# Kernel tuning notes

Measured on AMD Instinct MI355X. Metric: run time of the kernel, lower is better.

## Reference

```python
import jax, jax.numpy as jnp
import numpy as np

T, B, F, H = 128, 32768, 8, 64


def gru_step(h, x, Wih, Whh, bih, bhh):
    # PyTorch GRU cell, gate order (r, z, n)
    gi = x @ Wih.T + bih          # [B, 3H]
    gh = h @ Whh.T + bhh          # [B, 3H]
    i_r, i_z, i_n = jnp.split(gi, 3, axis=-1)
    h_r, h_z, h_n = jnp.split(gh, 3, axis=-1)
    r = jax.nn.sigmoid(i_r + h_r)
    z = jax.nn.sigmoid(i_z + h_z)
    n = jnp.tanh(i_n + r * h_n)
    return (1.0 - z) * n + z * h


def setup_inputs() -> dict:
    key = jax.random.key(0)
    ks = jax.random.split(key, 12)
    s = 0.1  # small init scale
    return {
        "inputs": jax.random.normal(ks[0], (T, B, F), jnp.float32),
        "target": jax.random.normal(ks[1], (T, B, F), jnp.float32),
        "enc_Wih": jax.random.normal(ks[2], (3 * H, F), jnp.float32) * s,
        "enc_Whh": jax.random.normal(ks[3], (3 * H, H), jnp.float32) * s,
        "enc_bih": jax.random.normal(ks[4], (3 * H,), jnp.float32) * s,
        "enc_bhh": jax.random.normal(ks[5], (3 * H,), jnp.float32) * s,
        "dec_Wih": jax.random.normal(ks[6], (3 * H, F), jnp.float32) * s,
        "dec_Whh": jax.random.normal(ks[7], (3 * H, H), jnp.float32) * s,
        "dec_bih": jax.random.normal(ks[8], (3 * H,), jnp.float32) * s,
        "dec_bhh": jax.random.normal(ks[9], (3 * H,), jnp.float32) * s,
        "out_W": jax.random.normal(ks[10], (F, H), jnp.float32) * s,
        "out_b": jax.random.normal(ks[11], (F,), jnp.float32) * s,
    }


def reference(inputs, target, enc_Wih, enc_Whh, enc_bih, enc_bhh,
              dec_Wih, dec_Whh, dec_bih, dec_bhh, out_W, out_b):
    batch = inputs.shape[1]
    # ---- Encoder: single-layer GRU over T steps, h0 = 0 ----
    h0 = jnp.zeros((batch, H), inputs.dtype)

    def enc_body(h, x_t):
        h = gru_step(h, x_t, enc_Wih, enc_Whh, enc_bih, enc_bhh)
        return h, None

    enc_hidden, _ = jax.lax.scan(enc_body, h0, inputs)

    # ---- Decoder: teacher forcing; input at t=0 is zeros, then target[t-1] ----
    dec_in = jnp.concatenate(
        [jnp.zeros((1, batch, target.shape[2]), target.dtype), target[:-1]], axis=0)

    def dec_body(h, x_t):
        h = gru_step(h, x_t, dec_Wih, dec_Whh, dec_bih, dec_bhh)
        y = h @ out_W.T + out_b  # [B, F]
        return h, y

    _, decoder_outputs = jax.lax.scan(dec_body, enc_hidden, dec_in)
    return decoder_outputs  # [T, B, F]
```

## Files before the change

### kernel.cpp

```cpp
#include <hip/hip_runtime.h>

#define T_STEPS 128
#define B_SIZE  32768
#define F_DIM   8
#define H_DIM   64

#define BLOCK_THREADS 128
#define GRID_BLOCKS   (B_SIZE / 16)

typedef float f32x4 __attribute__((ext_vector_type(4)));
typedef short bfrag __attribute__((ext_vector_type(8)));
typedef unsigned int u32x4 __attribute__((ext_vector_type(4)));

#define MFMA16(A, B, C) __builtin_amdgcn_mfma_f32_16x16x32_bf16((A), (B), (C), 0, 0, 0)

#define LDS_BARRIER() asm volatile("s_waitcnt lgkmcnt(0)\n\ts_barrier" ::: "memory")

__device__ __forceinline__ short f2bf(float f) { return __builtin_bit_cast(short, (__bf16)f); }
__device__ __forceinline__ float4 ld4(const void* p) { return *(const float4*)p; }

constexpr float S1 = 1.4426950408889634f;
constexpr float S2 = 2.f * S1;


__global__ void __launch_bounds__(BLOCK_THREADS, 2)
seq2seq_r9_kernel(const float* __restrict__ inputs, const float* __restrict__ target,
                  const float* __restrict__ eWih, const float* __restrict__ eWhh,
                  const float* __restrict__ ebih, const float* __restrict__ ebhh,
                  const float* __restrict__ dWih, const float* __restrict__ dWhh,
                  const float* __restrict__ dbih, const float* __restrict__ dbhh,
                  const float* __restrict__ oW, const float* __restrict__ ob,
                  float* __restrict__ out)
{
    __shared__ u32x4 sEx[2][2][64];

    const int tid  = threadIdx.x;
    const int lane = tid & 63;
    const int w    = tid >> 6;
    const int c    = lane & 15;
    const int g    = lane >> 4;

    bfrag wr[2][2], wz[2][2], whn[2][2];
    bfrag xr[2], xz[2], xnw[2];
    f32x4 bhn[2];

    auto load_phase = [&](const float* __restrict__ Wih, const float* __restrict__ Whh,
                          const float* __restrict__ bih, const float* __restrict__ bhh) {
#pragma unroll
        for (int tl = 0; tl < 2; ++tl) {
            const int tt = 2 * w + tl;
            const int rowR = 16 * tt + c, rowZ = rowR + 64, rowN = rowR + 128;
#pragma unroll
            for (int j = 0; j < 2; ++j) {
                const int kt = (j == 0) ? w : 1 - w;
                bfrag fr, fz, fn;
#pragma unroll
                for (int e = 0; e < 8; ++e) {
                    const int k = 32 * kt + 16 * (e >> 2) + 4 * g + (e & 3);
                    fr[e] = f2bf(Whh[rowR * H_DIM + k] * S1);
                    fz[e] = f2bf(Whh[rowZ * H_DIM + k] * S1);
                    fn[e] = f2bf(Whh[rowN * H_DIM + k] * S2);
                }
                wr[tl][j] = fr; wz[tl][j] = fz; whn[tl][j] = fn;
            }
            bfrag axr, axz, axn;
#pragma unroll
            for (int e = 0; e < 8; ++e) {
                const int k = 16 * (e >> 2) + 4 * g + (e & 3);
                float vr = 0.f, vz = 0.f, vn = 0.f;
                if (k < F_DIM) {
                    vr = Wih[rowR * F_DIM + k]; vz = Wih[rowZ * F_DIM + k]; vn = Wih[rowN * F_DIM + k];
                } else if (k == F_DIM) {
                    vr = bih[rowR] + bhh[rowR]; vz = bih[rowZ] + bhh[rowZ]; vn = bih[rowN];
                }
                axr[e] = f2bf(vr * S1); axz[e] = f2bf(vz * S1); axn[e] = f2bf(vn * S2);
            }
            xr[tl] = axr; xz[tl] = axz; xnw[tl] = axn;
#pragma unroll
            for (int r4 = 0; r4 < 4; ++r4) bhn[tl][r4] = bhh[128 + 16 * tt + 4 * g + r4] * S2;
        }
    };

    f32x4 hc[2] = {{0.f,0.f,0.f,0.f},{0.f,0.f,0.f,0.f}};
    bfrag hl = (bfrag){0,0,0,0,0,0,0,0};
    bfrag ho = (bfrag){0,0,0,0,0,0,0,0};
    bfrag bx0 = (bfrag){0,0,0,0,0,0,0,0};
    if (g == 2) bx0[0] = f2bf(1.f);

    auto step = [&](const bfrag bx) {
#pragma unroll
        for (int tl = 0; tl < 2; ++tl) {
            f32x4 aIN = {0.f,0.f,0.f,0.f};
            aIN = MFMA16(xnw[tl], bx, aIN);
            f32x4 aR = {0.f,0.f,0.f,0.f};
            aR = MFMA16(xr[tl], bx, aR);
            aR = MFMA16(wr[tl][0], hl, aR);
            f32x4 aZ = {0.f,0.f,0.f,0.f};
            aZ = MFMA16(xz[tl], bx, aZ);
            aZ = MFMA16(wz[tl][0], hl, aZ);
            f32x4 aHN = bhn[tl];
            aHN = MFMA16(whn[tl][0], hl, aHN);
            aR  = MFMA16(wr[tl][1],  ho, aR);
            aZ  = MFMA16(wz[tl][1],  ho, aZ);
            aHN = MFMA16(whn[tl][1], ho, aHN);
#pragma unroll
            for (int r4 = 0; r4 < 4; ++r4) {
                const float rg = __builtin_amdgcn_rcpf(1.f + __builtin_amdgcn_exp2f(-aR[r4]));
                const float zg = __builtin_amdgcn_rcpf(1.f + __builtin_amdgcn_exp2f(-aZ[r4]));
                const float np = aIN[r4] + rg * aHN[r4];
                const float ng = 1.f - 2.f * __builtin_amdgcn_rcpf(__builtin_amdgcn_exp2f(np) + 1.f);
                hc[tl][r4] = ng + zg * (hc[tl][r4] - ng);
            }
        }
        bfrag nl;
#pragma unroll
        for (int e = 0; e < 8; ++e) nl[e] = f2bf(hc[e >> 2][e & 3]);
        hl = nl;
    };

    auto make_bx = [&](const float4 xv) {
        bfrag bx = bx0;
        if (g < 2) { bx[0] = f2bf(xv.x); bx[1] = f2bf(xv.y); bx[2] = f2bf(xv.z); bx[3] = f2bf(xv.w); }
        return bx;
    };

    const unsigned istep = B_SIZE * F_DIM * 4;
    const unsigned off0  = ((unsigned)(blockIdx.x * 16 + c) * F_DIM + 4 * g) * 4;

    load_phase(eWih, eWhh, ebih, ebhh);
    __syncthreads();
    float4 xn = make_float4(0.f, 0.f, 0.f, 0.f);
    if (g < 2) xn = ld4((const char*)inputs + off0);
    unsigned ioff = off0 + istep;

    auto enc_body = [&](const int P, const int t) {
        const float4 xv = xn;
        if (g < 2 && t + 1 < T_STEPS) xn = ld4((const char*)inputs + ioff);
        ioff += istep;
        step(make_bx(xv));
        sEx[P][w][lane] = __builtin_bit_cast(u32x4, hl);
        LDS_BARRIER();
        ho = __builtin_bit_cast(bfrag, sEx[P][w ^ 1][lane]);
    };
#pragma unroll 1
    for (int t = 0; t < T_STEPS; t += 2) {
        enc_body(0, t);
        enc_body(1, t + 1);
    }

    load_phase(dWih, dWhh, dbih, dbhh);
    bfrag wo_own, wo_oth;
    f32x4 obv;
#pragma unroll
    for (int j = 0; j < 2; ++j) {
        bfrag f;
#pragma unroll
        for (int e = 0; e < 8; ++e) {
            const int k = 32 * ((j == 0) ? w : 1 - w) + 16 * (e >> 2) + 4 * g + (e & 3);
            f[e] = f2bf((c < F_DIM) ? oW[c * H_DIM + k] : 0.f);
        }
        if (j == 0) wo_own = f; else wo_oth = f;
    }
#pragma unroll
    for (int r4 = 0; r4 < 4; ++r4) obv[r4] = (g < 2) ? ob[4 * g + r4] : 0.f;

    unsigned toff = off0;
    unsigned ooff = off0;
    xn = make_float4(0.f, 0.f, 0.f, 0.f);

    auto dec_body = [&](const int P, const int t) {
        const float4 xv = xn;
        if (g < 2 && t + 1 < T_STEPS) xn = ld4((const char*)target + toff);
        toff += istep;
        step(make_bx(xv));
        sEx[P][w][lane] = __builtin_bit_cast(u32x4, hl);
        LDS_BARRIER();
        ho = __builtin_bit_cast(bfrag, sEx[P][w ^ 1][lane]);
        if (((t + w) & 1) == 0) {
            f32x4 aO = obv;
            aO = MFMA16(wo_own, hl, aO);
            aO = MFMA16(wo_oth, ho, aO);
            if (g < 2) {
                float4 o; o.x = aO[0]; o.y = aO[1]; o.z = aO[2]; o.w = aO[3];
                *(float4*)((char*)out + ooff) = o;
            }
        }
        ooff += istep;
    };
#pragma unroll 1
    for (int t = 0; t < T_STEPS; t += 2) {
        dec_body(0, t);
        dec_body(1, t + 1);
    }
}

extern "C" void kernel_launch(void* const* d_in, const int* in_sizes, int n_in,
                              void* d_out, int out_size, void* d_ws, size_t ws_size,
                              hipStream_t stream) {
    (void)in_sizes; (void)n_in; (void)d_ws; (void)ws_size; (void)out_size;
    const float* inputs = (const float*)d_in[0];
    const float* target = (const float*)d_in[1];
    const float* eWih   = (const float*)d_in[2];
    const float* eWhh   = (const float*)d_in[3];
    const float* ebih   = (const float*)d_in[4];
    const float* ebhh   = (const float*)d_in[5];
    const float* dWih   = (const float*)d_in[6];
    const float* dWhh   = (const float*)d_in[7];
    const float* dbih   = (const float*)d_in[8];
    const float* dbhh   = (const float*)d_in[9];
    const float* oW     = (const float*)d_in[10];
    const float* ob     = (const float*)d_in[11];
    float* out = (float*)d_out;

    seq2seq_r9_kernel<<<dim3(GRID_BLOCKS), dim3(BLOCK_THREADS), 0, stream>>>(
        inputs, target, eWih, eWhh, ebih, ebhh, dWih, dWhh, dbih, dbhh, oW, ob, out);
}
```

Before: 534.6 us.

## Split GRU gate rows across four waves, two batch groups per block

Each block now runs four waves over 32 batch rows in two groups. Each wave owns one 16-row gate tile of the hidden state and processes both batch groups, where before two waves each owned two tiles of a 16-row block. This halves the per-wave weight-fragment registers and interleaves two independent recurrence chains to hide MFMA and transcendental latency. The cost is a full 4-wave __syncthreads per step instead of a 2-wave barrier, and more LDS exchange traffic. The output-projection weights move to LDS and the output step rotates across waves.

```diff
diff --git a/kernel.cpp b/kernel.cpp
--- a/kernel.cpp
+++ b/kernel.cpp
@@ -5,16 +5,16 @@
 #define F_DIM   8
 #define H_DIM   64
 
-#define BLOCK_THREADS 128
-#define GRID_BLOCKS   (B_SIZE / 16)
+#define BLOCK_THREADS 256
+#define GRID_BLOCKS   (B_SIZE / 32)
 
 typedef float f32x4 __attribute__((ext_vector_type(4)));
 typedef short bfrag __attribute__((ext_vector_type(8)));
+typedef short s16x4 __attribute__((ext_vector_type(4)));
+typedef unsigned int u32x2 __attribute__((ext_vector_type(2)));
 typedef unsigned int u32x4 __attribute__((ext_vector_type(4)));
 
 #define MFMA16(A, B, C) __builtin_amdgcn_mfma_f32_16x16x32_bf16((A), (B), (C), 0, 0, 0)
-
-#define LDS_BARRIER() asm volatile("s_waitcnt lgkmcnt(0)\n\ts_barrier" ::: "memory")
 
 __device__ __forceinline__ short f2bf(float f) { return __builtin_bit_cast(short, (__bf16)f); }
 __device__ __forceinline__ float4 ld4(const void* p) { return *(const float4*)p; }
@@ -24,7 +24,7 @@
 
 
 __global__ void __launch_bounds__(BLOCK_THREADS, 2)
-seq2seq_r9_kernel(const float* __restrict__ inputs, const float* __restrict__ target,
+seq2seq_q4_kernel(const float* __restrict__ inputs, const float* __restrict__ target,
                   const float* __restrict__ eWih, const float* __restrict__ eWhh,
                   const float* __restrict__ ebih, const float* __restrict__ ebhh,
                   const float* __restrict__ dWih, const float* __restrict__ dWhh,
@@ -32,91 +32,56 @@
                   const float* __restrict__ oW, const float* __restrict__ ob,
                   float* __restrict__ out)
 {
-    __shared__ u32x4 sEx[2][2][64];
+    __shared__ u32x2 sEx[2][2][2][64][2];
+    __shared__ u32x4 sWo[2][64];
 
     const int tid  = threadIdx.x;
     const int lane = tid & 63;
-    const int w    = tid >> 6;
+    const int q    = tid >> 6;
     const int c    = lane & 15;
     const int g    = lane >> 4;
-
-    bfrag wr[2][2], wz[2][2], whn[2][2];
-    bfrag xr[2], xz[2], xnw[2];
-    f32x4 bhn[2];
+    const int kq   = q >> 1;
+    const int hq   = q & 1;
+
+    bfrag wr[2], wz[2], whn[2];
+    bfrag xr, xz, xnw;
+    f32x4 bhn;
 
     auto load_phase = [&](const float* __restrict__ Wih, const float* __restrict__ Whh,
                           const float* __restrict__ bih, const float* __restrict__ bhh) {
-#pragma unroll
-        for (int tl = 0; tl < 2; ++tl) {
-            const int tt = 2 * w + tl;
-            const int rowR = 16 * tt + c, rowZ = rowR + 64, rowN = rowR + 128;
-#pragma unroll
-            for (int j = 0; j < 2; ++j) {
-                const int kt = (j == 0) ? w : 1 - w;
-                bfrag fr, fz, fn;
-#pragma unroll
-                for (int e = 0; e < 8; ++e) {
-                    const int k = 32 * kt + 16 * (e >> 2) + 4 * g + (e & 3);
-                    fr[e] = f2bf(Whh[rowR * H_DIM + k] * S1);
-                    fz[e] = f2bf(Whh[rowZ * H_DIM + k] * S1);
-                    fn[e] = f2bf(Whh[rowN * H_DIM + k] * S2);
-                }
-                wr[tl][j] = fr; wz[tl][j] = fz; whn[tl][j] = fn;
+        const int rowR = 16 * q + c, rowZ = rowR + 64, rowN = rowR + 128;
+#pragma unroll
+        for (int kt = 0; kt < 2; ++kt) {
+            bfrag fr, fz, fn;
+#pragma unroll
+            for (int e = 0; e < 8; ++e) {
+                const int k = 32 * kt + 16 * (e >> 2) + 4 * g + (e & 3);
+                fr[e] = f2bf(Whh[rowR * H_DIM + k] * S1);
+                fz[e] = f2bf(Whh[rowZ * H_DIM + k] * S1);
+                fn[e] = f2bf(Whh[rowN * H_DIM + k] * S2);
             }
-            bfrag axr, axz, axn;
-#pragma unroll
-            for (int e = 0; e < 8; ++e) {
-                const int k = 16 * (e >> 2) + 4 * g + (e & 3);
-                float vr = 0.f, vz = 0.f, vn = 0.f;
-                if (k < F_DIM) {
-                    vr = Wih[rowR * F_DIM + k]; vz = Wih[rowZ * F_DIM + k]; vn = Wih[rowN * F_DIM + k];
-                } else if (k == F_DIM) {
-                    vr = bih[rowR] + bhh[rowR]; vz = bih[rowZ] + bhh[rowZ]; vn = bih[rowN];
-                }
-                axr[e] = f2bf(vr * S1); axz[e] = f2bf(vz * S1); axn[e] = f2bf(vn * S2);
+            wr[kt] = fr; wz[kt] = fz; whn[kt] = fn;
+        }
+#pragma unroll
+        for (int e = 0; e < 8; ++e) {
+            const int k = 16 * (e >> 2) + 4 * g + (e & 3);
+            float vr = 0.f, vz = 0.f, vn = 0.f;
+            if (k < F_DIM) {
+                vr = Wih[rowR * F_DIM + k]; vz = Wih[rowZ * F_DIM + k]; vn = Wih[rowN * F_DIM + k];
+            } else if (k == F_DIM) {
+                vr = bih[rowR] + bhh[rowR]; vz = bih[rowZ] + bhh[rowZ]; vn = bih[rowN];
             }
-            xr[tl] = axr; xz[tl] = axz; xnw[tl] = axn;
-#pragma unroll
-            for (int r4 = 0; r4 < 4; ++r4) bhn[tl][r4] = bhh[128 + 16 * tt + 4 * g + r4] * S2;
-        }
+            xr[e] = f2bf(vr * S1); xz[e] = f2bf(vz * S1); xnw[e] = f2bf(vn * S2);
+        }
+#pragma unroll
+        for (int r4 = 0; r4 < 4; ++r4) bhn[r4] = bhh[128 + 16 * q + 4 * g + r4] * S2;
     };
 
     f32x4 hc[2] = {{0.f,0.f,0.f,0.f},{0.f,0.f,0.f,0.f}};
-    bfrag hl = (bfrag){0,0,0,0,0,0,0,0};
-    bfrag ho = (bfrag){0,0,0,0,0,0,0,0};
+    bfrag hB[2][2] = {{(bfrag){0,0,0,0,0,0,0,0},(bfrag){0,0,0,0,0,0,0,0}},
+                      {(bfrag){0,0,0,0,0,0,0,0},(bfrag){0,0,0,0,0,0,0,0}}};
     bfrag bx0 = (bfrag){0,0,0,0,0,0,0,0};
     if (g == 2) bx0[0] = f2bf(1.f);
-
-    auto step = [&](const bfrag bx) {
-#pragma unroll
-        for (int tl = 0; tl < 2; ++tl) {
-            f32x4 aIN = {0.f,0.f,0.f,0.f};
-            aIN = MFMA16(xnw[tl], bx, aIN);
-            f32x4 aR = {0.f,0.f,0.f,0.f};
-            aR = MFMA16(xr[tl], bx, aR);
-            aR = MFMA16(wr[tl][0], hl, aR);
-            f32x4 aZ = {0.f,0.f,0.f,0.f};
-            aZ = MFMA16(xz[tl], bx, aZ);
-            aZ = MFMA16(wz[tl][0], hl, aZ);
-            f32x4 aHN = bhn[tl];
-            aHN = MFMA16(whn[tl][0], hl, aHN);
-            aR  = MFMA16(wr[tl][1],  ho, aR);
-            aZ  = MFMA16(wz[tl][1],  ho, aZ);
-            aHN = MFMA16(whn[tl][1], ho, aHN);
-#pragma unroll
-            for (int r4 = 0; r4 < 4; ++r4) {
-                const float rg = __builtin_amdgcn_rcpf(1.f + __builtin_amdgcn_exp2f(-aR[r4]));
-                const float zg = __builtin_amdgcn_rcpf(1.f + __builtin_amdgcn_exp2f(-aZ[r4]));
-                const float np = aIN[r4] + rg * aHN[r4];
-                const float ng = 1.f - 2.f * __builtin_amdgcn_rcpf(__builtin_amdgcn_exp2f(np) + 1.f);
-                hc[tl][r4] = ng + zg * (hc[tl][r4] - ng);
-            }
-        }
-        bfrag nl;
-#pragma unroll
-        for (int e = 0; e < 8; ++e) nl[e] = f2bf(hc[e >> 2][e & 3]);
-        hl = nl;
-    };
 
     auto make_bx = [&](const float4 xv) {
         bfrag bx = bx0;
@@ -124,23 +89,59 @@
         return bx;
     };
 
+    auto step = [&](const bfrag bx, const bfrag hB0, const bfrag hB1, f32x4& HC) -> u32x2 {
+        f32x4 aIN = {0.f,0.f,0.f,0.f};
+        aIN = MFMA16(xnw, bx, aIN);
+        f32x4 aR = {0.f,0.f,0.f,0.f};
+        aR = MFMA16(xr, bx, aR);
+        aR = MFMA16(wr[0], hB0, aR);
+        aR = MFMA16(wr[1], hB1, aR);
+        f32x4 aZ = {0.f,0.f,0.f,0.f};
+        aZ = MFMA16(xz, bx, aZ);
+        aZ = MFMA16(wz[0], hB0, aZ);
+        aZ = MFMA16(wz[1], hB1, aZ);
+        f32x4 aHN = bhn;
+        aHN = MFMA16(whn[0], hB0, aHN);
+        aHN = MFMA16(whn[1], hB1, aHN);
+        s16x4 nb;
+#pragma unroll
+        for (int r4 = 0; r4 < 4; ++r4) {
+            const float rg = __builtin_amdgcn_rcpf(1.f + __builtin_amdgcn_exp2f(-aR[r4]));
+            const float zg = __builtin_amdgcn_rcpf(1.f + __builtin_amdgcn_exp2f(-aZ[r4]));
+            const float np = aIN[r4] + rg * aHN[r4];
+            const float ng = 1.f - 2.f * __builtin_amdgcn_rcpf(__builtin_amdgcn_exp2f(np) + 1.f);
+            HC[r4] = ng + zg * (HC[r4] - ng);
+            nb[r4] = f2bf(HC[r4]);
+        }
+        return __builtin_bit_cast(u32x2, nb);
+    };
+
     const unsigned istep = B_SIZE * F_DIM * 4;
-    const unsigned off0  = ((unsigned)(blockIdx.x * 16 + c) * F_DIM + 4 * g) * 4;
+    const unsigned offg[2] = {
+        ((unsigned)(blockIdx.x * 32 + c) * F_DIM + 4 * g) * 4u,
+        ((unsigned)(blockIdx.x * 32 + 16 + c) * F_DIM + 4 * g) * 4u };
 
     load_phase(eWih, eWhh, ebih, ebhh);
     __syncthreads();
-    float4 xn = make_float4(0.f, 0.f, 0.f, 0.f);
-    if (g < 2) xn = ld4((const char*)inputs + off0);
-    unsigned ioff = off0 + istep;
+    float4 xn[2] = {make_float4(0.f,0.f,0.f,0.f), make_float4(0.f,0.f,0.f,0.f)};
+    if (g < 2) { xn[0] = ld4((const char*)inputs + offg[0]); xn[1] = ld4((const char*)inputs + offg[1]); }
+    unsigned ioff = istep;
 
     auto enc_body = [&](const int P, const int t) {
-        const float4 xv = xn;
-        if (g < 2 && t + 1 < T_STEPS) xn = ld4((const char*)inputs + ioff);
+#pragma unroll
+        for (int grp = 0; grp < 2; ++grp) {
+            const float4 xv = xn[grp];
+            if (g < 2 && t + 1 < T_STEPS) xn[grp] = ld4((const char*)inputs + ioff + offg[grp]);
+            const u32x2 nl = step(make_bx(xv), hB[grp][0], hB[grp][1], hc[grp]);
+            sEx[P][grp][kq][lane][hq] = nl;
+        }
         ioff += istep;
-        step(make_bx(xv));
-        sEx[P][w][lane] = __builtin_bit_cast(u32x4, hl);
-        LDS_BARRIER();
-        ho = __builtin_bit_cast(bfrag, sEx[P][w ^ 1][lane]);
+        __syncthreads();
+#pragma unroll
+        for (int grp = 0; grp < 2; ++grp) {
+            hB[grp][0] = __builtin_bit_cast(bfrag, *(const u32x4*)&sEx[P][grp][0][lane][0]);
+            hB[grp][1] = __builtin_bit_cast(bfrag, *(const u32x4*)&sEx[P][grp][1][lane][0]);
+        }
     };
 #pragma unroll 1
     for (int t = 0; t < T_STEPS; t += 2) {
@@ -148,41 +149,55 @@
         enc_body(1, t + 1);
     }
 
+    __syncthreads();
     load_phase(dWih, dWhh, dbih, dbhh);
-    bfrag wo_own, wo_oth;
+    if (q < 2) {
+        u32x4 f;
+        bfrag bf_;
+#pragma unroll
+        for (int e = 0; e < 8; ++e) {
+            const int k = 32 * q + 16 * (e >> 2) + 4 * g + (e & 3);
+            bf_[e] = f2bf((c < F_DIM) ? oW[c * H_DIM + k] : 0.f);
+        }
+        f = __builtin_bit_cast(u32x4, bf_);
+        sWo[q][lane] = f;
+    }
     f32x4 obv;
 #pragma unroll
-    for (int j = 0; j < 2; ++j) {
-        bfrag f;
-#pragma unroll
-        for (int e = 0; e < 8; ++e) {
-            const int k = 32 * ((j == 0) ? w : 1 - w) + 16 * (e >> 2) + 4 * g + (e & 3);
-            f[e] = f2bf((c < F_DIM) ? oW[c * H_DIM + k] : 0.f);
-        }
-        if (j == 0) wo_own = f; else wo_oth = f;
-    }
-#pragma unroll
     for (int r4 = 0; r4 < 4; ++r4) obv[r4] = (g < 2) ? ob[4 * g + r4] : 0.f;
-
-    unsigned toff = off0;
-    unsigned ooff = off0;
-    xn = make_float4(0.f, 0.f, 0.f, 0.f);
+    __syncthreads();
+
+    unsigned toff = 0;
+    unsigned ooff = 0;
+    xn[0] = xn[1] = make_float4(0.f, 0.f, 0.f, 0.f);
 
     auto dec_body = [&](const int P, const int t) {
-        const float4 xv = xn;
-        if (g < 2 && t + 1 < T_STEPS) xn = ld4((const char*)target + toff);
+#pragma unroll
+        for (int grp = 0; grp < 2; ++grp) {
+            const float4 xv = xn[grp];
+            if (g < 2 && t + 1 < T_STEPS) xn[grp] = ld4((const char*)target + toff + offg[grp]);
+            const u32x2 nl = step(make_bx(xv), hB[grp][0], hB[grp][1], hc[grp]);
+            sEx[P][grp][kq][lane][hq] = nl;
+        }
         toff += istep;
-        step(make_bx(xv));
-        sEx[P][w][lane] = __builtin_bit_cast(u32x4, hl);
-        LDS_BARRIER();
-        ho = __builtin_bit_cast(bfrag, sEx[P][w ^ 1][lane]);
-        if (((t + w) & 1) == 0) {
-            f32x4 aO = obv;
-            aO = MFMA16(wo_own, hl, aO);
-            aO = MFMA16(wo_oth, ho, aO);
-            if (g < 2) {
-                float4 o; o.x = aO[0]; o.y = aO[1]; o.z = aO[2]; o.w = aO[3];
-                *(float4*)((char*)out + ooff) = o;
+        __syncthreads();
+#pragma unroll
+        for (int grp = 0; grp < 2; ++grp) {
+            hB[grp][0] = __builtin_bit_cast(bfrag, *(const u32x4*)&sEx[P][grp][0][lane][0]);
+            hB[grp][1] = __builtin_bit_cast(bfrag, *(const u32x4*)&sEx[P][grp][1][lane][0]);
+        }
+        if ((t & 3) == q) {
+            const bfrag wo0 = __builtin_bit_cast(bfrag, sWo[0][lane]);
+            const bfrag wo1 = __builtin_bit_cast(bfrag, sWo[1][lane]);
+#pragma unroll
+            for (int grp = 0; grp < 2; ++grp) {
+                f32x4 aO = obv;
+                aO = MFMA16(wo0, hB[grp][0], aO);
+                aO = MFMA16(wo1, hB[grp][1], aO);
+                if (g < 2) {
+                    float4 o; o.x = aO[0]; o.y = aO[1]; o.z = aO[2]; o.w = aO[3];
+                    *(float4*)((char*)out + ooff + offg[grp]) = o;
+                }
             }
         }
         ooff += istep;
@@ -212,6 +227,6 @@
     const float* ob     = (const float*)d_in[11];
     float* out = (float*)d_out;
 
-    seq2seq_r9_kernel<<<dim3(GRID_BLOCKS), dim3(BLOCK_THREADS), 0, stream>>>(
+    seq2seq_q4_kernel<<<dim3(GRID_BLOCKS), dim3(BLOCK_THREADS), 0, stream>>>(
         inputs, target, eWih, eWhh, ebih, ebhh, dWih, dWhh, dbih, dbhh, oW, ob, out);
 }
```

Measured after the change: 483.4 us. 9.6% less time.
